# Performance work log

Measured on AMD Instinct MI355X. Metric: run time of the kernel, lower is better.

Reference implementation:

```python
import jax, jax.numpy as jnp
import numpy as np

N, E = 50000, 800000
DIM, H, D = 256, 16, 8          # dim, num_heads, qk_dim
DH = D * H                      # 128
IN_RPE = 18
SCALE = D ** -0.5               # default qk_scale (None -> 1/sqrt(qk_dim))
EPS = 1e-16                     # torch_geometric softmax denominator eps


def setup_inputs() -> dict:
    key = jax.random.key(0)
    ks = jax.random.split(key, 10)
    x = jax.random.normal(ks[0], (N, DIM), dtype=jnp.float32)
    edge_index = jax.random.randint(ks[1], (2, E), 0, N, dtype=jnp.int64)
    edge_attr = jax.random.normal(ks[2], (E, IN_RPE), dtype=jnp.float32)
    # qkv Linear(dim -> 2*D*H + dim)
    Wqkv = jax.random.normal(ks[3], (DIM, 2 * DH + DIM), dtype=jnp.float32) * DIM ** -0.5
    bqkv = jnp.zeros((2 * DH + DIM,), dtype=jnp.float32)
    # k_rpe / q_rpe Linear(in_rpe_dim -> D*H) (heads_share_rpe=False)
    Wk_rpe = jax.random.normal(ks[4], (IN_RPE, DH), dtype=jnp.float32) * IN_RPE ** -0.5
    bk_rpe = jnp.zeros((DH,), dtype=jnp.float32)
    Wq_rpe = jax.random.normal(ks[5], (IN_RPE, DH), dtype=jnp.float32) * IN_RPE ** -0.5
    bq_rpe = jnp.zeros((DH,), dtype=jnp.float32)
    return {"x": x, "edge_index": edge_index, "edge_attr": edge_attr,
            "Wqkv": Wqkv, "bqkv": bqkv,
            "Wk_rpe": Wk_rpe, "bk_rpe": bk_rpe,
            "Wq_rpe": Wq_rpe, "bq_rpe": bq_rpe}


def _segment_softmax(compat, s, num_nodes):
    # numerically-stable softmax over edges grouped by source node s; compat: (E,H)
    m = jax.ops.segment_max(compat, s, num_segments=num_nodes)   # (N,H)
    ex = jnp.exp(compat - m[s])
    den = jax.ops.segment_sum(ex, s, num_segments=num_nodes)     # (N,H)
    return ex / (den[s] + EPS)


def reference(x, edge_index, edge_attr, Wqkv, bqkv, Wk_rpe, bk_rpe, Wq_rpe, bq_rpe):
    n = x.shape[0]
    e = edge_index.shape[1]
    qkv = x @ Wqkv + bqkv                      # (N, 2*DH + DIM)
    q = qkv[:, :DH].reshape(n, H, D)
    k = qkv[:, DH:2 * DH].reshape(n, H, D)
    v = qkv[:, 2 * DH:].reshape(n, H, DIM // H)
    s, t = edge_index[0], edge_index[1]
    qe = q[s] * SCALE                          # (E,H,D)
    ke = k[t]
    ke = ke + (edge_attr @ Wk_rpe + bk_rpe).reshape(e, H, D)
    qe = qe + (edge_attr @ Wq_rpe + bq_rpe).reshape(e, H, D)
    compat = jnp.einsum('ehd,ehd->eh', qe, ke)  # (E,H)
    attn = _segment_softmax(compat, s, n)       # (E,H)
    msg = (v[t] * attn[..., None]).reshape(e, DIM)  # (E,DIM)
    out = jax.ops.segment_sum(msg, s, num_segments=n)  # (N,DIM)
    return out
```

## Files before the change

kernel.cpp:

```cpp
#include <hip/hip_runtime.h>
#include <math.h>

#define DIMX   256
#define HEADS  16
#define QKD    8
#define DH     128
#define QKVW   512
#define INRPE  18
#define SCALE  0.35355339059327373f

typedef __attribute__((ext_vector_type(8))) short bf16x8;
typedef __attribute__((ext_vector_type(4))) float f32x4;

__device__ __forceinline__ void split1(float v, unsigned short& h, unsigned short& l)
{
    unsigned b  = __float_as_uint(v);
    unsigned hb = (b + 0x7FFFu + ((b >> 16) & 1u)) & 0xFFFF0000u;
    h = (unsigned short)(hb >> 16);
    float r = v - __uint_as_float(hb);
    unsigned rb = __float_as_uint(r);
    l = (unsigned short)((rb + 0x7FFFu + ((rb >> 16) & 1u)) >> 16);
}

__global__ __launch_bounds__(256) void convert_x(
    const float* __restrict__ x, unsigned short* __restrict__ xh,
    unsigned short* __restrict__ xl, int Nn, int Mpad)
{
    size_t total = (size_t)Mpad * 64;
    for (size_t i = (size_t)blockIdx.x * blockDim.x + threadIdx.x; i < total;
         i += (size_t)gridDim.x * blockDim.x) {
        size_t row = i >> 6;
        float4 v = make_float4(0.f, 0.f, 0.f, 0.f);
        if (row < (size_t)Nn) v = *(const float4*)&x[i * 4];
        ushort4 h, l;
        split1(v.x, h.x, l.x);
        split1(v.y, h.y, l.y);
        split1(v.z, h.z, l.z);
        split1(v.w, h.w, l.w);
        *(ushort4*)&xh[i * 4] = h;
        *(ushort4*)&xl[i * 4] = l;
    }
}

__global__ __launch_bounds__(256) void convert_w(
    const float* __restrict__ W, unsigned short* __restrict__ wth,
    unsigned short* __restrict__ wtl)
{
    int n = blockIdx.x;
    int k = threadIdx.x;
    float v = W[(size_t)k * QKVW + n];
    unsigned short h, l;
    split1(v, h, l);
    wth[(size_t)n * DIMX + k] = h;
    wtl[(size_t)n * DIMX + k] = l;
}

__global__ __launch_bounds__(256, 2) void qkv_gemm_mfma(
    const unsigned short* __restrict__ xh, const unsigned short* __restrict__ xl,
    const unsigned short* __restrict__ wth, const unsigned short* __restrict__ wtl,
    const float* __restrict__ bias, float* __restrict__ qkv, int Nn)
{
    int tid  = threadIdx.x;
    int w    = tid >> 6, lane = tid & 63;
    int wm   = w >> 1,   wn   = w & 1;
    int row0 = blockIdx.x * 128 + wm * 64;
    int col0 = blockIdx.y * 128 + wn * 64;
    int lrow = lane & 15;
    int lk8  = (lane >> 4) * 8;

    const unsigned short* pah = xh  + (size_t)(row0 + lrow) * DIMX + lk8;
    const unsigned short* pal = xl  + (size_t)(row0 + lrow) * DIMX + lk8;
    const unsigned short* pbh = wth + (size_t)(col0 + lrow) * DIMX + lk8;
    const unsigned short* pbl = wtl + (size_t)(col0 + lrow) * DIMX + lk8;

    f32x4 acc[4][4];
    #pragma unroll
    for (int i = 0; i < 4; i++)
        #pragma unroll
        for (int j = 0; j < 4; j++)
            acc[i][j] = (f32x4){0.f, 0.f, 0.f, 0.f};

    for (int t = 0; t < DIMX / 32; ++t) {
        int kb = t * 32;
        bf16x8 ah[4], al[4], bh[4], bl[4];
        #pragma unroll
        for (int f = 0; f < 4; ++f) {
            ah[f] = *(const bf16x8*)(pah + (size_t)f * 4096 + kb);
            al[f] = *(const bf16x8*)(pal + (size_t)f * 4096 + kb);
            bh[f] = *(const bf16x8*)(pbh + (size_t)f * 4096 + kb);
            bl[f] = *(const bf16x8*)(pbl + (size_t)f * 4096 + kb);
        }
        #pragma unroll
        for (int fm = 0; fm < 4; ++fm)
            #pragma unroll
            for (int fn = 0; fn < 4; ++fn) {
                acc[fm][fn] = __builtin_amdgcn_mfma_f32_16x16x32_bf16(
                    ah[fm], bh[fn], acc[fm][fn], 0, 0, 0);
                acc[fm][fn] = __builtin_amdgcn_mfma_f32_16x16x32_bf16(
                    ah[fm], bl[fn], acc[fm][fn], 0, 0, 0);
                acc[fm][fn] = __builtin_amdgcn_mfma_f32_16x16x32_bf16(
                    al[fm], bh[fn], acc[fm][fn], 0, 0, 0);
            }
    }

    float sc = (blockIdx.y == 0) ? SCALE : 1.0f;
    int rbase = (lane >> 4) * 4;
    #pragma unroll
    for (int fn = 0; fn < 4; ++fn) {
        float bv = bias[col0 + fn * 16 + lrow];
        #pragma unroll
        for (int fm = 0; fm < 4; ++fm) {
            #pragma unroll
            for (int j = 0; j < 4; ++j) {
                int r = row0 + fm * 16 + rbase + j;
                if (r < Nn)
                    qkv[(size_t)r * QKVW + col0 + fn * 16 + lrow] =
                        (acc[fm][fn][j] + bv) * sc;
            }
        }
    }
}

__global__ __launch_bounds__(256) void qkv_gemm(
    const float* __restrict__ x, const float* __restrict__ W,
    const float* __restrict__ bias, float* __restrict__ qkv, int Nn)
{
    __shared__ float As[16][132];
    __shared__ float Bs[16][132];

    int tid  = threadIdx.x;
    int row0 = blockIdx.x * 128;
    int col0 = blockIdx.y * 128;
    int tx = tid & 15, ty = tid >> 4;

    float acc[8][8] = {};

    for (int k0 = 0; k0 < DIMX; k0 += 16) {
        #pragma unroll
        for (int r = 0; r < 2; r++) {
            int idx  = tid + r * 256;
            int arow = idx >> 2, acol = (idx & 3) * 4;
            float4 av = make_float4(0.f, 0.f, 0.f, 0.f);
            int grow = row0 + arow;
            if (grow < Nn) av = *(const float4*)&x[(size_t)grow * DIMX + k0 + acol];
            As[acol + 0][arow] = av.x;
            As[acol + 1][arow] = av.y;
            As[acol + 2][arow] = av.z;
            As[acol + 3][arow] = av.w;
        }
        #pragma unroll
        for (int r = 0; r < 2; r++) {
            int idx  = tid + r * 256;
            int brow = idx >> 5, bcol = (idx & 31) * 4;
            float4 bv = *(const float4*)&W[(size_t)(k0 + brow) * QKVW + col0 + bcol];
            *(float4*)&Bs[brow][bcol] = bv;
        }
        __syncthreads();
        #pragma unroll
        for (int kk = 0; kk < 16; kk++) {
            float a0[8], b0[8];
            *(float4*)&a0[0] = *(const float4*)&As[kk][ty * 8];
            *(float4*)&a0[4] = *(const float4*)&As[kk][ty * 8 + 4];
            *(float4*)&b0[0] = *(const float4*)&Bs[kk][tx * 4];
            *(float4*)&b0[4] = *(const float4*)&Bs[kk][64 + tx * 4];
            #pragma unroll
            for (int i = 0; i < 8; i++)
                #pragma unroll
                for (int j = 0; j < 8; j++)
                    acc[i][j] = fmaf(a0[i], b0[j], acc[i][j]);
        }
        __syncthreads();
    }

    float4 bv0 = *(const float4*)&bias[col0 + tx * 4];
    float4 bv1 = *(const float4*)&bias[col0 + 64 + tx * 4];
    float sc = (col0 == 0) ? SCALE : 1.0f;
    #pragma unroll
    for (int i = 0; i < 8; i++) {
        int grow = row0 + ty * 8 + i;
        if (grow < Nn) {
            float4 o0, o1;
            o0.x = (acc[i][0] + bv0.x) * sc;
            o0.y = (acc[i][1] + bv0.y) * sc;
            o0.z = (acc[i][2] + bv0.z) * sc;
            o0.w = (acc[i][3] + bv0.w) * sc;
            o1.x = (acc[i][4] + bv1.x) * sc;
            o1.y = (acc[i][5] + bv1.y) * sc;
            o1.z = (acc[i][6] + bv1.z) * sc;
            o1.w = (acc[i][7] + bv1.w) * sc;
            *(float4*)&qkv[(size_t)grow * QKVW + col0 + tx * 4] = o0;
            *(float4*)&qkv[(size_t)grow * QKVW + col0 + 64 + tx * 4] = o1;
        }
    }
}

__global__ void count_kernel(const int* __restrict__ ei, int* __restrict__ deg, int E)
{
    int e = blockIdx.x * blockDim.x + threadIdx.x;
    if (e < E) atomicAdd(&deg[ei[e]], 1);
}

__global__ __launch_bounds__(1024) void scan_kernel(
    const int* __restrict__ deg, int* __restrict__ off, int n)
{
    __shared__ int wsum[16];
    __shared__ int wbase[16];
    __shared__ int tot;
    int tid = threadIdx.x;
    int lane = tid & 63, w = tid >> 6;
    int carry = 0;
    for (int base = 0; base < n; base += 1024) {
        int idx = base + tid;
        int v = (idx < n) ? deg[idx] : 0;
        int acc = v;
        #pragma unroll
        for (int d = 1; d < 64; d <<= 1) {
            int u = __shfl_up(acc, d, 64);
            if (lane >= d) acc += u;
        }
        if (lane == 63) wsum[w] = acc;
        __syncthreads();
        if (tid < 16) {
            int s = wsum[tid];
            int a = s;
            #pragma unroll
            for (int d = 1; d < 16; d <<= 1) {
                int u = __shfl_up(a, d, 64);
                if (tid >= d) a += u;
            }
            wbase[tid] = a - s;
            if (tid == 15) tot = a;
        }
        __syncthreads();
        if (idx < n) off[idx] = carry + wbase[w] + (acc - v);
        carry += tot;
        __syncthreads();
    }
    if (tid == 0) off[n] = carry;
}

__global__ void scatter_kernel(const int* __restrict__ ei,
                               const int* __restrict__ off, int* __restrict__ cur,
                               int2* __restrict__ elist, int E)
{
    int e = blockIdx.x * blockDim.x + threadIdx.x;
    if (e < E) {
        int s = ei[e];
        int t = ei[E + e];
        int pos = atomicAdd(&cur[s], 1);
        elist[off[s] + pos] = make_int2(e, t);
    }
}

__global__ __launch_bounds__(128, 3) void node_attn(
    const float* __restrict__ qkv, const int2* __restrict__ elist,
    const int* __restrict__ off, const float* __restrict__ edge_attr,
    const float* __restrict__ Wq_rpe, const float* __restrict__ bq_rpe,
    const float* __restrict__ Wk_rpe, const float* __restrict__ bk_rpe,
    float* __restrict__ out, int Nn)
{
    int tid = threadIdx.x;
    int n = blockIdx.x;
    if (n >= Nn) return;

    float wq[INRPE], wk[INRPE];
    #pragma unroll
    for (int j = 0; j < INRPE; j++) {
        wq[j] = *(volatile const float*)&Wq_rpe[j * DH + tid];
        wk[j] = *(volatile const float*)&Wk_rpe[j * DH + tid];
    }
    float qs = qkv[(size_t)n * QKVW + tid] + bq_rpe[tid];
    float bk = bk_rpe[tid];

    int beg = off[n], end = off[n + 1];

    float lsum = 0.0f;
    float2 o = make_float2(0.f, 0.f);

    int2 etn = (beg < end) ? elist[beg] : make_int2(0, 0);

    #pragma unroll 2
    for (int i = beg; i < end; i++) {
        int2 et = etn;
        if (i + 1 < end) etn = elist[i + 1];
        int e = et.x, t = et.y;

        float  kt = qkv[(size_t)t * QKVW + DH + tid];
        float2 vt = *(const float2*)&qkv[(size_t)t * QKVW + 2 * DH + 2 * tid];

        const float2* ea2 = (const float2*)(edge_attr + (size_t)e * INRPE);
        float qr = 0.f, kr = bk;
        #pragma unroll
        for (int j = 0; j < 9; j++) {
            float2 av = ea2[j];
            qr = fmaf(av.x, wq[2 * j], qr);
            kr = fmaf(av.x, wk[2 * j], kr);
            qr = fmaf(av.y, wq[2 * j + 1], qr);
            kr = fmaf(av.y, wk[2 * j + 1], kr);
        }

        float c2 = (qs + qr) * (kt + kr);
        c2 += __shfl_xor(c2, 1, 64);
        c2 += __shfl_xor(c2, 2, 64);
        c2 += __shfl_xor(c2, 4, 64);

        float ex = __expf(c2);
        lsum += ex;
        o.x = fmaf(ex, vt.x, o.x);
        o.y = fmaf(ex, vt.y, o.y);
    }

    float inv = 1.0f / (lsum + 1e-16f);
    *(float2*)&out[(size_t)n * DIMX + 2 * tid] = make_float2(o.x * inv, o.y * inv);
}

extern "C" void kernel_launch(void* const* d_in, const int* in_sizes, int n_in,
                              void* d_out, int out_size, void* d_ws, size_t ws_size,
                              hipStream_t stream)
{
    const float* x    = (const float*)d_in[0];
    const int*   ei   = (const int*)d_in[1];
    const float* ea   = (const float*)d_in[2];
    const float* Wqkv = (const float*)d_in[3];
    const float* bqkv = (const float*)d_in[4];
    const float* Wk   = (const float*)d_in[5];
    const float* bk   = (const float*)d_in[6];
    const float* Wq   = (const float*)d_in[7];
    const float* bq   = (const float*)d_in[8];

    int Nn = in_sizes[0] / DIMX;
    int E  = in_sizes[1] / 2;
    float* out = (float*)d_out;

    int Mblocks = (Nn + 127) / 128;
    int Mpad    = Mblocks * 128;

    size_t qkv_bytes  = (size_t)Nn * QKVW * sizeof(float);
    float* qkv = (float*)d_ws;
    char*  P   = (char*)d_ws + qkv_bytes;

    size_t xpart  = (size_t)Mpad * DIMX * sizeof(unsigned short);
    size_t wpart  = (size_t)QKVW * DIMX * sizeof(unsigned short);
    size_t gemm_bytes = 2 * xpart + 2 * wpart;
    size_t csr_bytes  = sizeof(int) * (size_t)(3 * Nn + 2) + sizeof(int2) * (size_t)E;
    size_t need = qkv_bytes + (gemm_bytes > csr_bytes ? gemm_bytes : csr_bytes);

    int*  deg = (int*)P;
    int*  cur = deg + Nn;
    int*  off = cur + Nn;
    int2* elist = (int2*)(off + ((Nn + 2) & ~1));

    if (ws_size >= need) {
        unsigned short* xh  = (unsigned short*)P;
        unsigned short* xl  = xh + (size_t)Mpad * DIMX;
        unsigned short* wth = xl + (size_t)Mpad * DIMX;
        unsigned short* wtl = wth + (size_t)QKVW * DIMX;

        convert_x<<<2048, 256, 0, stream>>>(x, xh, xl, Nn, Mpad);
        convert_w<<<QKVW, 256, 0, stream>>>(Wqkv, wth, wtl);
        qkv_gemm_mfma<<<dim3(Mblocks, 4), 256, 0, stream>>>(xh, xl, wth, wtl,
                                                            bqkv, qkv, Nn);
    } else {
        qkv_gemm<<<dim3(Mblocks, QKVW / 128), 256, 0, stream>>>(x, Wqkv, bqkv, qkv, Nn);
    }

    hipMemsetAsync(deg, 0, sizeof(int) * 2 * (size_t)Nn, stream);
    count_kernel<<<(E + 255) / 256, 256, 0, stream>>>(ei, deg, E);
    scan_kernel<<<1, 1024, 0, stream>>>(deg, off, Nn);
    scatter_kernel<<<(E + 255) / 256, 256, 0, stream>>>(ei, off, cur, elist, E);
    node_attn<<<Nn, 128, 0, stream>>>(qkv, elist, off, ea, Wq, bq, Wk, bk, out, Nn);
}
```

Measured before the change: 673.4 us.

## Software-pipeline edge gathers in node_attn with two-stage prefetch

Restructures the per-node edge loop so the k/v rows and edge attributes of the next edge are loaded while the current edge is computed, and edge indices are prefetched two ahead. The volatile weight loads become normal loads pinned in registers with an empty asm barrier, and nodes with no edges write zeros and return early. This is meant to hide gather latency in a memory-latency-bound loop. In exchange it uses more registers, so the occupancy hint is lowered from 3 to 2 blocks per CU, which could cost latency hiding.

```diff
diff --git a/kernel.cpp b/kernel.cpp
--- a/kernel.cpp
+++ b/kernel.cpp
@@ -252,7 +252,7 @@
     }
 }
 
-__global__ __launch_bounds__(128, 3) void node_attn(
+__global__ __launch_bounds__(128, 2) void node_attn(
     const float* __restrict__ qkv, const int2* __restrict__ elist,
     const int* __restrict__ off, const float* __restrict__ edge_attr,
     const float* __restrict__ Wq_rpe, const float* __restrict__ bq_rpe,
@@ -266,48 +266,72 @@
     float wq[INRPE], wk[INRPE];
     #pragma unroll
     for (int j = 0; j < INRPE; j++) {
-        wq[j] = *(volatile const float*)&Wq_rpe[j * DH + tid];
-        wk[j] = *(volatile const float*)&Wk_rpe[j * DH + tid];
-    }
+        wq[j] = Wq_rpe[j * DH + tid];
+        wk[j] = Wk_rpe[j * DH + tid];
+    }
+    #pragma unroll
+    for (int j = 0; j < INRPE; j++) {
+        asm volatile("" : "+v"(wq[j]), "+v"(wk[j]));
+    }
+
     float qs = qkv[(size_t)n * QKVW + tid] + bq_rpe[tid];
     float bk = bk_rpe[tid];
 
     int beg = off[n], end = off[n + 1];
 
+    if (beg == end) {
+        *(float2*)&out[(size_t)n * DIMX + 2 * tid] = make_float2(0.f, 0.f);
+        return;
+    }
+
     float lsum = 0.0f;
     float2 o = make_float2(0.f, 0.f);
 
-    int2 etn = (beg < end) ? elist[beg] : make_int2(0, 0);
-
-    #pragma unroll 2
+    int2 etc = elist[beg];
+    float  ktc = qkv[(size_t)etc.y * QKVW + DH + tid];
+    float2 vtc = *(const float2*)&qkv[(size_t)etc.y * QKVW + 2 * DH + 2 * tid];
+    float eac[INRPE];
+    {
+        const float2* p = (const float2*)(edge_attr + (size_t)etc.x * INRPE);
+        #pragma unroll
+        for (int j = 0; j < 9; j++) { float2 v2 = p[j]; eac[2*j] = v2.x; eac[2*j+1] = v2.y; }
+    }
+    int2 etn = elist[(beg + 1 < end) ? beg + 1 : beg];
+
+    #pragma unroll 1
     for (int i = beg; i < end; i++) {
-        int2 et = etn;
-        if (i + 1 < end) etn = elist[i + 1];
-        int e = et.x, t = et.y;
-
-        float  kt = qkv[(size_t)t * QKVW + DH + tid];
-        float2 vt = *(const float2*)&qkv[(size_t)t * QKVW + 2 * DH + 2 * tid];
-
-        const float2* ea2 = (const float2*)(edge_attr + (size_t)e * INRPE);
+        int inx2 = (i + 2 < end) ? i + 2 : end - 1;
+        int2 et2 = elist[inx2];
+        float  ktn = qkv[(size_t)etn.y * QKVW + DH + tid];
+        float2 vtn = *(const float2*)&qkv[(size_t)etn.y * QKVW + 2 * DH + 2 * tid];
+        float ean[INRPE];
+        {
+            const float2* p = (const float2*)(edge_attr + (size_t)etn.x * INRPE);
+            #pragma unroll
+            for (int j = 0; j < 9; j++) { float2 v2 = p[j]; ean[2*j] = v2.x; ean[2*j+1] = v2.y; }
+        }
+
         float qr = 0.f, kr = bk;
         #pragma unroll
-        for (int j = 0; j < 9; j++) {
-            float2 av = ea2[j];
-            qr = fmaf(av.x, wq[2 * j], qr);
-            kr = fmaf(av.x, wk[2 * j], kr);
-            qr = fmaf(av.y, wq[2 * j + 1], qr);
-            kr = fmaf(av.y, wk[2 * j + 1], kr);
-        }
-
-        float c2 = (qs + qr) * (kt + kr);
+        for (int j = 0; j < INRPE; j++) {
+            qr = fmaf(eac[j], wq[j], qr);
+            kr = fmaf(eac[j], wk[j], kr);
+        }
+
+        float c2 = (qs + qr) * (ktc + kr);
         c2 += __shfl_xor(c2, 1, 64);
         c2 += __shfl_xor(c2, 2, 64);
         c2 += __shfl_xor(c2, 4, 64);
 
         float ex = __expf(c2);
         lsum += ex;
-        o.x = fmaf(ex, vt.x, o.x);
-        o.y = fmaf(ex, vt.y, o.y);
+        o.x = fmaf(ex, vtc.x, o.x);
+        o.y = fmaf(ex, vtc.y, o.y);
+
+        etc = etn; etn = et2;
+        ktc = ktn; vtc = vtn;
+        #pragma unroll
+        for (int j = 0; j < INRPE; j++) eac[j] = ean[j];
     }
 
     float inv = 1.0f / (lsum + 1e-16f);
```

Measured after the change: 613.8 us. 1.1x faster.
